# Performance work log

Measured on AMD Instinct MI355X. Metric: run time of the kernel, lower is better.

Reference implementation:

```python
import jax, jax.numpy as jnp
import numpy as np

ATT = 64   # attention_size (becomes number of split chunks / effective heads)
NH = 16    # num_heads (becomes chunk width / effective head dim)


def setup_inputs() -> dict:
    key = jax.random.key(0)
    ks = jax.random.split(key, 9)
    B, T, E = 4, 1024, 1024
    AH = ATT * NH  # 1024
    s = 0.02
    return {
        "x": jax.random.normal(ks[0], (B, T, E), jnp.float32),
        "Wq": jax.random.normal(ks[1], (E, AH), jnp.float32) * s,
        "bq": jax.random.normal(ks[2], (AH,), jnp.float32) * s,
        "Wk": jax.random.normal(ks[3], (E, AH), jnp.float32) * s,
        "bk": jax.random.normal(ks[4], (AH,), jnp.float32) * s,
        "Wv": jax.random.normal(ks[5], (E, AH), jnp.float32) * s,
        "bv": jax.random.normal(ks[6], (AH,), jnp.float32) * s,
        "Wo": jax.random.normal(ks[7], (AH, E), jnp.float32) * s,
        "bo": jax.random.normal(ks[8], (E,), jnp.float32) * s,
    }


def reference(x, Wq, bq, Wk, bk, Wv, bv, Wo, bo):
    B, T, E = x.shape
    A, H = ATT, NH

    q = x @ Wq + bq  # [B,T,A*H]
    k = x @ Wk + bk
    v = x @ Wv + bv

    # torch.split(m, num_heads, dim=2) -> A chunks of width H; cat along dim 0
    def split_cat(m):
        # [B,T,A,H] -> [A,B,T,H] -> [A*B,T,H]
        return m.reshape(B, T, A, H).transpose(2, 0, 1, 3).reshape(A * B, T, H)

    q = split_cat(q)
    k = split_cat(k)
    v = split_cat(v)

    scores = jnp.einsum('bqh,bkh->bqk', q, k) / (A ** 0.5)  # [A*B,T,T]
    attn = jax.nn.softmax(scores, axis=-1)
    z = jnp.einsum('bqk,bkh->bqh', attn, v)  # [A*B,T,H]

    # faithful to torch: contiguous [A*B,T,H] viewed as [B, T, A*H] (no un-permute)
    z = z.reshape(B, T, A * H)
    return z @ Wo + bo
```

## Files before the change

### kernel.cpp

```cpp
#include <hip/hip_runtime.h>
#include <hip/hip_bf16.h>


typedef __bf16 bf16_t;
typedef bf16_t bf16x8 __attribute__((ext_vector_type(8)));
typedef bf16_t bf16x4 __attribute__((ext_vector_type(4)));
typedef short  s16x4 __attribute__((ext_vector_type(4)));
typedef float  f32x4 __attribute__((ext_vector_type(4)));

#define SCALE_LOG2E 0.18033688011112042f

__device__ __forceinline__ void async16(const bf16_t* g, void* l) {
    __builtin_amdgcn_global_load_lds(
        (const __attribute__((address_space(1))) unsigned int*)g,
        (__attribute__((address_space(3))) unsigned int*)l,
        16, 0, 0);
}

__global__ __launch_bounds__(256) void cast_f32_bf16(
    const float* __restrict__ in, bf16_t* __restrict__ out, int n8)
{
    int i = blockIdx.x * 256 + threadIdx.x;
    if (i >= n8) return;
    const float4* p = (const float4*)in + (size_t)i * 2;
    float4 a = p[0], b = p[1];
    bf16x8 o;
    o[0] = (bf16_t)a.x; o[1] = (bf16_t)a.y; o[2] = (bf16_t)a.z; o[3] = (bf16_t)a.w;
    o[4] = (bf16_t)b.x; o[5] = (bf16_t)b.y; o[6] = (bf16_t)b.z; o[7] = (bf16_t)b.w;
    *((bf16x8*)out + i) = o;
}

__global__ __launch_bounds__(256) void transpose_cast(
    const float* __restrict__ W0, const float* __restrict__ W1,
    const float* __restrict__ W2, const float* __restrict__ W3,
    bf16_t* __restrict__ out)
{
    __shared__ float st[32][33];
    const float* W = (blockIdx.z == 0) ? W0 : (blockIdx.z == 1) ? W1
                   : (blockIdx.z == 2) ? W2 : W3;
    bf16_t* o = out + (size_t)blockIdx.z * 1024 * 1024;
    const int n0 = blockIdx.x * 32, k0 = blockIdx.y * 32;
    const int t = threadIdx.x;
    const int r = t >> 3, c4 = (t & 7) * 4;
    float4 v = *(const float4*)(W + (size_t)(k0 + r) * 1024 + n0 + c4);
    st[r][c4 + 0] = v.x; st[r][c4 + 1] = v.y; st[r][c4 + 2] = v.z; st[r][c4 + 3] = v.w;
    __syncthreads();
    bf16_t tmp[4] __attribute__((aligned(8)));
    #pragma unroll
    for (int i = 0; i < 4; ++i) tmp[i] = (bf16_t)st[c4 + i][r];
    *(uint2*)(o + (size_t)(n0 + r) * 1024 + k0 + c4) = *(const uint2*)tmp;
}

template<bool FUSED, int MT>
__global__ __launch_bounds__(256, 3) void gemm_glds(
    const bf16_t* __restrict__ A, const bf16_t* __restrict__ Bt,
    const float* __restrict__ b0, const float* __restrict__ b1,
    const float* __restrict__ b2,
    bf16_t* __restrict__ Qo, bf16_t* __restrict__ Ko, bf16_t* __restrict__ Vo,
    float* __restrict__ Fo)
{
    const int K = 1024;
    __shared__ __align__(16) bf16_t As[2 * MT * 32];
    __shared__ __align__(16) bf16_t Bs[2 * 128 * 32];

    constexpr int NTPW = (MT == 128) ? 4 : 2;
    constexpr int JA   = MT / 64;
    constexpr int NX   = FUSED ? 24 : 8;
    constexpr int NWG  = NX * ((MT == 128) ? 32 : 64);

    const int tid  = threadIdx.x;
    const int wave = tid >> 6;
    const int lane = tid & 63;
    const int quad = lane >> 4;
    const int l16  = lane & 15;

    int flat = blockIdx.y * NX + blockIdx.x;
    flat = (flat & 7) * (NWG >> 3) + (flat >> 3);
    const int m0 = (flat / NX) * MT;
    const int n0 = (flat % NX) * 128;

    const int wm = (MT == 128) ? (wave >> 1) * 64 : 0;
    const int wn = (MT == 128) ? (wave & 1) * 64 : wave * 32;

    int goffA[JA], goffB[2];
    #pragma unroll
    for (int j = 0; j < JA; ++j) {
        const int row = j * 64 + (tid >> 2);
        const int cl  = (tid & 3) ^ ((row >> 1) & 3);
        goffA[j] = (m0 + row) * K + cl * 8;
    }
    #pragma unroll
    for (int j = 0; j < 2; ++j) {
        const int row = j * 64 + (tid >> 2);
        const int cl  = (tid & 3) ^ ((row >> 1) & 3);
        goffB[j] = (n0 + row) * K + cl * 8;
    }
    const int ldsoff = wave * 1024;

    f32x4 acc[4][NTPW] = {};
    const int sw = (l16 >> 1) & 3;

    for (int k0 = 0; k0 < K; k0 += 64) {
        #pragma unroll
        for (int s = 0; s < 2; ++s) {
            #pragma unroll
            for (int j = 0; j < JA; ++j)
                async16(A + goffA[j] + k0 + s * 32,
                        (char*)As + s * (MT * 64) + j * 4096 + ldsoff);
            #pragma unroll
            for (int j = 0; j < 2; ++j)
                async16(Bt + goffB[j] + k0 + s * 32,
                        (char*)Bs + s * 8192 + j * 4096 + ldsoff);
        }
        __syncthreads();

        #pragma unroll
        for (int s = 0; s < 2; ++s) {
            bf16x8 af[4], bfr[NTPW];
            #pragma unroll
            for (int mt = 0; mt < 4; ++mt)
                af[mt] = *(const bf16x8*)(&As[s * (MT * 32) +
                    (wm + mt * 16 + l16) * 32 + (quad ^ sw) * 8]);
            #pragma unroll
            for (int nt = 0; nt < NTPW; ++nt)
                bfr[nt] = *(const bf16x8*)(&Bs[s * (128 * 32) +
                    (wn + nt * 16 + l16) * 32 + (quad ^ sw) * 8]);
            #pragma unroll
            for (int mt = 0; mt < 4; ++mt)
                #pragma unroll
                for (int nt = 0; nt < NTPW; ++nt)
                    acc[mt][nt] = __builtin_amdgcn_mfma_f32_16x16x32_bf16(
                        af[mt], bfr[nt], acc[mt][nt], 0, 0, 0);
        }
        __syncthreads();
    }

    if (FUSED) {
        const int sel = n0 >> 10;
        const float* bias = (sel == 0) ? b0 : (sel == 1) ? b1 : b2;
        bf16_t* Cout      = (sel == 0) ? Qo : (sel == 1) ? Ko : Vo;
        const float scl   = (sel == 1) ? SCALE_LOG2E : 1.0f;
        const int nb = n0 & 1023;
        #pragma unroll
        for (int nt = 0; nt < NTPW; ++nt) {
            const int n = nb + wn + nt * 16 + l16;
            const float bb = bias[n];
            const size_t hbase = (size_t)(n >> 4) * 65536 + (n & 15);
            #pragma unroll
            for (int mt = 0; mt < 4; ++mt)
                #pragma unroll
                for (int i = 0; i < 4; ++i) {
                    const int m = m0 + wm + mt * 16 + quad * 4 + i;
                    Cout[hbase + (size_t)m * 16] = (bf16_t)((acc[mt][nt][i] + bb) * scl);
                }
        }
    } else {
        #pragma unroll
        for (int nt = 0; nt < NTPW; ++nt) {
            const int n = n0 + wn + nt * 16 + l16;
            const float bb = b0[n];
            #pragma unroll
            for (int mt = 0; mt < 4; ++mt)
                #pragma unroll
                for (int i = 0; i < 4; ++i) {
                    const int m = m0 + wm + mt * 16 + quad * 4 + i;
                    Fo[(size_t)m * 1024 + n] = acc[mt][nt][i] + bb;
                }
        }
    }
}

__global__ __launch_bounds__(512, 4) void attn_kernel(
    const bf16_t* __restrict__ Q, const bf16_t* __restrict__ K,
    const bf16_t* __restrict__ V, bf16_t* __restrict__ Z)
{
    __shared__ __align__(16) char smem[16 * 1032 * 2];
    bf16_t (*Vt)[1032] = (bf16_t (*)[1032])smem;
    float* cmb = (float*)smem;

    const int tid  = threadIdx.x;
    const int wave = tid >> 6;
    const int lane = tid & 63;
    const int quad = lane >> 4;
    const int l16  = lane & 15;
    const int hd = blockIdx.x >> 2;
    const int qc = blockIdx.x & 3;
    const int a = hd >> 2, b = hd & 3;
    const int qw   = wave & 3;
    const int kvh  = wave >> 2;
    const int qbase = qc * 256 + qw * 64;
    const int kb512 = kvh * 512;

    const size_t hb = (size_t)a * 65536 + (size_t)b * 1024 * 16;

    const int r  = tid >> 2;
    const int dq = (tid & 3) * 4;
    const bf16_t* Vp = V + hb + (size_t)r * 16 + dq;
    #pragma unroll 2
    for (int t = 0; t < 8; ++t) {
        uint2 vv = *(const uint2*)(Vp + t * 2048);
        bf16_t t4[4] __attribute__((aligned(8)));
        *(uint2*)t4 = vv;
        #pragma unroll
        for (int ii = 0; ii < 4; ++ii)
            Vt[dq + ii][t * 128 + r] = t4[ii];
    }

    bf16x8 qf[4] = {};
    if (quad < 2) {
        #pragma unroll
        for (int qs = 0; qs < 4; ++qs)
            qf[qs] = *(const bf16x8*)(Q + hb +
                (size_t)(qbase + qs * 16 + l16) * 16 + quad * 8);
    }

    const bf16_t* Kp = K + hb + (size_t)(kb512 + l16) * 16 + quad * 8;
    bf16x8 kfA[4] = {}, kfB[4] = {};
    if (quad < 2) {
        #pragma unroll
        for (int kt = 0; kt < 4; ++kt)
            kfA[kt] = *(const bf16x8*)(Kp + kt * 256);
    }

    __syncthreads();

    const s16x4 ones = { 0x3F80, 0x3F80, 0x3F80, 0x3F80 };

    f32x4 zacc[4] = {};
    f32x4 lacc[4] = {};

#define ATTN_TILE(JIDX, KFCUR, KFNXT, DO_PREFETCH)                            \
    {                                                                         \
        const int j_ = (JIDX);                                                \
        if (DO_PREFETCH && quad < 2) {                                        \
            _Pragma("unroll")                                                 \
            for (int kt = 0; kt < 4; ++kt)                                    \
                KFNXT[kt] = *(const bf16x8*)(                                 \
                    Kp + (j_ + 1) * 1024 + kt * 256);                         \
        }                                                                     \
        _Pragma("unroll")                                                     \
        for (int kt = 0; kt < 4; ++kt) {                                      \
            const s16x4 vfrag = __builtin_bit_cast(s16x4,                     \
                *(const uint2*)(&Vt[l16][kb512 + j_ * 64 + kt * 16 + quad * 4])); \
            _Pragma("unroll")                                                 \
            for (int qs = 0; qs < 4; ++qs) {                                  \
                f32x4 zc = {0.f, 0.f, 0.f, 0.f};                              \
                f32x4 s = __builtin_amdgcn_mfma_f32_16x16x32_bf16(            \
                    KFCUR[kt], qf[qs], zc, 0, 0, 0);                          \
                const float e0 = __builtin_amdgcn_exp2f(s[0]);                \
                const float e1 = __builtin_amdgcn_exp2f(s[1]);                \
                const float e2 = __builtin_amdgcn_exp2f(s[2]);                \
                const float e3 = __builtin_amdgcn_exp2f(s[3]);                \
                bf16x4 pv;                                                    \
                pv[0] = (bf16_t)e0; pv[1] = (bf16_t)e1;                       \
                pv[2] = (bf16_t)e2; pv[3] = (bf16_t)e3;                       \
                const s16x4 pfrag = __builtin_bit_cast(s16x4, pv);            \
                zacc[qs] = __builtin_amdgcn_mfma_f32_16x16x16bf16_1k(         \
                    vfrag, pfrag, zacc[qs], 0, 0, 0);                         \
                lacc[qs] = __builtin_amdgcn_mfma_f32_16x16x16bf16_1k(         \
                    ones, pfrag, lacc[qs], 0, 0, 0);                          \
            }                                                                 \
        }                                                                     \
    }

    #pragma unroll 1
    for (int j2 = 0; j2 < 4; ++j2) {
        ATTN_TILE(2 * j2,     kfA, kfB, true)
        ATTN_TILE(2 * j2 + 1, kfB, kfA, (j2 < 3))
    }
#undef ATTN_TILE

    __syncthreads();
    if (wave >= 4) {
        float* p = cmb + ((size_t)((wave - 4) * 64 + lane)) * 21;
        #pragma unroll
        for (int qs = 0; qs < 4; ++qs) {
            #pragma unroll
            for (int i = 0; i < 4; ++i) p[qs * 4 + i] = zacc[qs][i];
            p[16 + qs] = lacc[qs][0];
        }
    }
    __syncthreads();
    if (wave < 4) {
        const float* p = cmb + ((size_t)(wave * 64 + lane)) * 21;
        #pragma unroll
        for (int qs = 0; qs < 4; ++qs) {
            const float inv = 1.0f / (lacc[qs][0] + p[16 + qs]);
            const int q = qbase + qs * 16 + l16;
            bf16_t o4[4] __attribute__((aligned(8)));
            #pragma unroll
            for (int i = 0; i < 4; ++i)
                o4[i] = (bf16_t)((zacc[qs][i] + p[qs * 4 + i]) * inv);
            *(uint2*)(Z + ((size_t)hd * 1024 + q) * 16 + quad * 4) = *(const uint2*)o4;
        }
    }
}

extern "C" void kernel_launch(void* const* d_in, const int* in_sizes, int n_in,
                              void* d_out, int out_size, void* d_ws, size_t ws_size,
                              hipStream_t stream) {
    const float* x  = (const float*)d_in[0];
    const float* Wq = (const float*)d_in[1];
    const float* bq = (const float*)d_in[2];
    const float* Wk = (const float*)d_in[3];
    const float* bk = (const float*)d_in[4];
    const float* Wv = (const float*)d_in[5];
    const float* bv = (const float*)d_in[6];
    const float* Wo = (const float*)d_in[7];
    const float* bo = (const float*)d_in[8];
    float* out = (float*)d_out;

    char* ws = (char*)d_ws;
    bf16_t* x_bf = (bf16_t*)(ws);
    bf16_t* Wt   = (bf16_t*)(ws + (8u << 20));
    bf16_t* Qb   = (bf16_t*)(ws + (16u << 20));
    bf16_t* Kb   = (bf16_t*)(ws + (24u << 20));
    bf16_t* Vb   = (bf16_t*)(ws + (32u << 20));
    bf16_t* Zb   = (bf16_t*)(ws + (40u << 20));
    bf16_t* WtO  = Wt + (size_t)3 * 1024 * 1024;

    cast_f32_bf16<<<dim3(2048), dim3(256), 0, stream>>>(x, x_bf, 524288);
    transpose_cast<<<dim3(32, 32, 4), dim3(256), 0, stream>>>(Wq, Wk, Wv, Wo, Wt);

    gemm_glds<true, 128><<<dim3(24, 32), dim3(256), 0, stream>>>(
        x_bf, Wt, bq, bk, bv, Qb, Kb, Vb, nullptr);

    attn_kernel<<<dim3(1024), dim3(512), 0, stream>>>(Qb, Kb, Vb, Zb);

    gemm_glds<false, 64><<<dim3(8, 64), dim3(256), 0, stream>>>(
        Zb, WtO, bo, nullptr, nullptr, nullptr, nullptr, nullptr, out);
}
```

Baseline: 180.7 us.

## Add split-K output projection GEMM with two wave groups and LDS reduction

Replaces the generic output-projection GEMM with a dedicated 512-thread kernel in which two groups of four waves each handle half of the K dimension. The partial sums are combined through shared memory before bias is added and the result stored. The aim is more waves per tile and better latency hiding on the 4096x1024x1024 projection. In exchange it adds an LDS reduction step and a heavier per-block footprint.

Result: slower. 190.5 us (+5.4%).

```diff
diff --git a/kernel.cpp b/kernel.cpp
--- a/kernel.cpp
+++ b/kernel.cpp
@@ -165,6 +165,109 @@
                 for (int i = 0; i < 4; ++i) {
                     const int m = m0 + wm + mt * 16 + quad * 4 + i;
                     Fo[(size_t)m * 1024 + n] = acc[mt][nt][i] + bb;
+                }
+        }
+    }
+}
+
+__global__ __launch_bounds__(512, 4) void gemm_oproj(
+    const bf16_t* __restrict__ A, const bf16_t* __restrict__ Bt,
+    const float* __restrict__ bias, float* __restrict__ Fo)
+{
+    __shared__ __align__(16) char smem[49152];
+    bf16_t* As  = (bf16_t*)smem;
+    bf16_t* Bs  = (bf16_t*)(smem + 16384);
+    float*  cmb = (float*)smem;
+
+    const int K = 1024;
+    const int tid  = threadIdx.x;
+    const int wave = tid >> 6;
+    const int grp  = wave >> 2;
+    const int qw   = wave & 3;
+    const int lane = tid & 63;
+    const int quad = lane >> 4;
+    const int l16  = lane & 15;
+    const int tl   = tid & 255;
+
+    int flat = blockIdx.y * 8 + blockIdx.x;
+    flat = (flat & 7) * 64 + (flat >> 3);
+    const int m0 = (flat >> 3) * 64;
+    const int n0 = (flat & 7) * 128;
+    const int wn = qw * 32;
+    const int kb = grp * 512;
+
+    const int rowA  = tl >> 2;
+    const int clA   = (tl & 3) ^ ((rowA >> 1) & 3);
+    const int goffA = (m0 + rowA) * K + kb + clA * 8;
+    int goffB[2];
+    #pragma unroll
+    for (int j = 0; j < 2; ++j) {
+        const int row = j * 64 + (tl >> 2);
+        const int cl  = (tl & 3) ^ ((row >> 1) & 3);
+        goffB[j] = (n0 + row) * K + kb + cl * 8;
+    }
+    const int ldsoffq = qw * 1024;
+
+    f32x4 acc[4][2] = {};
+    const int sw = (l16 >> 1) & 3;
+
+    for (int k0 = 0; k0 < 512; k0 += 64) {
+        #pragma unroll
+        for (int s = 0; s < 2; ++s) {
+            async16(A + goffA + k0 + s * 32,
+                    (char*)As + grp * 8192 + s * 4096 + ldsoffq);
+            #pragma unroll
+            for (int j = 0; j < 2; ++j)
+                async16(Bt + goffB[j] + k0 + s * 32,
+                        (char*)Bs + grp * 16384 + s * 8192 + j * 4096 + ldsoffq);
+        }
+        __syncthreads();
+
+        #pragma unroll
+        for (int s = 0; s < 2; ++s) {
+            bf16x8 af[4], bfr[2];
+            #pragma unroll
+            for (int mt = 0; mt < 4; ++mt)
+                af[mt] = *(const bf16x8*)(&As[grp * 4096 + s * 2048 +
+                    (mt * 16 + l16) * 32 + (quad ^ sw) * 8]);
+            #pragma unroll
+            for (int nt = 0; nt < 2; ++nt)
+                bfr[nt] = *(const bf16x8*)(&Bs[grp * 8192 + s * 4096 +
+                    (wn + nt * 16 + l16) * 32 + (quad ^ sw) * 8]);
+            #pragma unroll
+            for (int mt = 0; mt < 4; ++mt)
+                #pragma unroll
+                for (int nt = 0; nt < 2; ++nt)
+                    acc[mt][nt] = __builtin_amdgcn_mfma_f32_16x16x32_bf16(
+                        af[mt], bfr[nt], acc[mt][nt], 0, 0, 0);
+        }
+        __syncthreads();
+    }
+
+    if (grp == 1) {
+        float* p = cmb + ((size_t)(qw * 64 + lane)) * 32;
+        #pragma unroll
+        for (int mt = 0; mt < 4; ++mt)
+            #pragma unroll
+            for (int nt = 0; nt < 2; ++nt)
+                #pragma unroll
+                for (int i = 0; i < 4; ++i)
+                    p[mt * 8 + nt * 4 + i] = acc[mt][nt][i];
+    }
+    __syncthreads();
+    if (grp == 0) {
+        const float* p = cmb + ((size_t)(qw * 64 + lane)) * 32;
+        #pragma unroll
+        for (int nt = 0; nt < 2; ++nt) {
+            const int n = n0 + wn + nt * 16 + l16;
+            const float bb = bias[n];
+            #pragma unroll
+            for (int mt = 0; mt < 4; ++mt)
+                #pragma unroll
+                for (int i = 0; i < 4; ++i) {
+                    const int m = m0 + mt * 16 + quad * 4 + i;
+                    Fo[(size_t)m * 1024 + n] =
+                        acc[mt][nt][i] + p[mt * 8 + nt * 4 + i] + bb;
                 }
         }
     }
@@ -327,6 +430,5 @@
 
     attn_kernel<<<dim3(1024), dim3(512), 0, stream>>>(Qb, Kb, Vb, Zb);
 
-    gemm_glds<false, 64><<<dim3(8, 64), dim3(256), 0, stream>>>(
-        Zb, WtO, bo, nullptr, nullptr, nullptr, nullptr, nullptr, out);
-}
+    gemm_oproj<<<dim3(8, 64), dim3(512), 0, stream>>>(Zb, WtO, bo, out);
+}
```
